# Kernel tuning notes

Measured on AMD Instinct MI355X. Metric: run time of the kernel, lower is better.

Reference implementation:

```python
import jax, jax.numpy as jnp
import numpy as np

R = 32          # voxel resolution (init kwarg)
EPS = 0.0       # init kwarg eps


def _norm_coords(coords):
    # coords: [B, 3, N]
    nc = coords - coords.mean(axis=2, keepdims=True)
    # L2 norm over xyz (dim=1), max over points (dim=2)
    denom = jnp.linalg.norm(nc, axis=1, keepdims=True).max(axis=2, keepdims=True) * 2.0 + EPS
    nc = nc / denom + 0.5
    return jnp.clip(nc * R, 0.0, R - 1)  # [B, 3, N] in [0, R-1]


def setup_inputs() -> dict:
    key = jax.random.key(0)
    k1, k2 = jax.random.split(key)
    features = jax.random.normal(k1, (8, 64, 65536), dtype=jnp.float32)
    coords = jax.random.normal(k2, (8, 3, 65536), dtype=jnp.float32)
    return {"features": features, "coords": coords}


def reference(features, coords):
    # features: [B, C, N], coords: [B, 3, N]
    nc = _norm_coords(coords)
    vox = jnp.round(nc).astype(jnp.int32)                      # [B, 3, N]
    flat = (vox[:, 0] * R + vox[:, 1]) * R + vox[:, 2]         # [B, N] flat voxel ids

    def per_batch(f, idx):
        # f: [C, N], idx: [N] -> scatter-mean into R^3 voxels
        sums = jax.ops.segment_sum(f.T, idx, num_segments=R ** 3)            # [R^3, C]
        cnt = jax.ops.segment_sum(jnp.ones(idx.shape, jnp.float32), idx,
                                  num_segments=R ** 3)                        # [R^3]
        return (sums / jnp.maximum(cnt, 1.0)[:, None]).T                      # [C, R^3]

    vox_feat = jax.vmap(per_batch)(features, flat)             # [B, C, R^3]
    B, C = features.shape[0], features.shape[1]
    return vox_feat.reshape(B, C, R, R, R), nc
```

## Files before the change

kernel.cpp:

```cpp
#include <hip/hip_runtime.h>

#define RR 32
#define R3 32768
#define NPTS 65536
#define NCH 64
#define NB 8


__global__ void mean_kernel(const float* __restrict__ coords, double* __restrict__ sums) {
    int b = blockIdx.y;
    int tid = blockIdx.x * blockDim.x + threadIdx.x;
    int stride = gridDim.x * blockDim.x;
    const float* cb = coords + (size_t)b * 3 * NPTS;
    double sx = 0.0, sy = 0.0, sz = 0.0;
    for (int n = tid; n < NPTS; n += stride) {
        sx += cb[n];
        sy += cb[NPTS + n];
        sz += cb[2 * NPTS + n];
    }
    for (int off = 32; off > 0; off >>= 1) {
        sx += __shfl_down(sx, off);
        sy += __shfl_down(sy, off);
        sz += __shfl_down(sz, off);
    }
    if ((threadIdx.x & 63) == 0) {
        atomicAdd(&sums[b * 3 + 0], sx);
        atomicAdd(&sums[b * 3 + 1], sy);
        atomicAdd(&sums[b * 3 + 2], sz);
    }
}

__global__ void maxnorm_kernel(const float* __restrict__ coords,
                               const double* __restrict__ sums,
                               unsigned* __restrict__ maxbits) {
    int b = blockIdx.y;
    float mx = (float)(sums[b * 3 + 0] * (1.0 / NPTS));
    float my = (float)(sums[b * 3 + 1] * (1.0 / NPTS));
    float mz = (float)(sums[b * 3 + 2] * (1.0 / NPTS));
    int tid = blockIdx.x * blockDim.x + threadIdx.x;
    int stride = gridDim.x * blockDim.x;
    const float* cb = coords + (size_t)b * 3 * NPTS;
    float m = 0.0f;
    for (int n = tid; n < NPTS; n += stride) {
        float dx = cb[n] - mx;
        float dy = cb[NPTS + n] - my;
        float dz = cb[2 * NPTS + n] - mz;
        m = fmaxf(m, dx * dx + dy * dy + dz * dz);
    }
    for (int off = 32; off > 0; off >>= 1) {
        m = fmaxf(m, __shfl_down(m, off));
    }
    if ((threadIdx.x & 63) == 0) {
        atomicMax(&maxbits[b], __float_as_uint(m));
    }
}


__global__ void scatter_vm_kernel(const float* __restrict__ feats,
                                  const float* __restrict__ coords,
                                  const double* __restrict__ sums,
                                  const unsigned* __restrict__ maxbits,
                                  float* __restrict__ ws_vox,
                                  float* __restrict__ ncout,
                                  float* __restrict__ cnt) {
    __shared__ float tile[64][65];
    __shared__ int   sflat[64];

    int b  = blockIdx.y;
    int n0 = blockIdx.x * 64;
    int t  = threadIdx.x;

    if (t < 64) {
        int n = n0 + t;
        float mx = (float)(sums[b * 3 + 0] * (1.0 / NPTS));
        float my = (float)(sums[b * 3 + 1] * (1.0 / NPTS));
        float mz = (float)(sums[b * 3 + 2] * (1.0 / NPTS));
        float denom = 2.0f * sqrtf(__uint_as_float(maxbits[b]));
        const float* cb = coords + (size_t)b * 3 * NPTS;
        float dx = cb[n] - mx;
        float dy = cb[NPTS + n] - my;
        float dz = cb[2 * NPTS + n] - mz;
        float qx = fminf(fmaxf((dx / denom + 0.5f) * 32.0f, 0.0f), 31.0f);
        float qy = fminf(fmaxf((dy / denom + 0.5f) * 32.0f, 0.0f), 31.0f);
        float qz = fminf(fmaxf((dz / denom + 0.5f) * 32.0f, 0.0f), 31.0f);
        float* nb_ = ncout + (size_t)b * 3 * NPTS;
        nb_[n] = qx;
        nb_[NPTS + n] = qy;
        nb_[2 * NPTS + n] = qz;
        int flat = ((int)rintf(qx) * RR + (int)rintf(qy)) * RR + (int)rintf(qz);
        sflat[t] = flat;
        atomicAdd(&cnt[b * R3 + flat], 1.0f);
    }

    const float* fb = feats + (size_t)b * NCH * NPTS + n0;
    int i = t & 63;
    int c0 = t >> 6;
#pragma unroll
    for (int iter = 0; iter < 16; iter++) {
        int c = iter * 4 + c0;
        tile[i][c] = fb[(size_t)c * NPTS + i];
    }
    __syncthreads();

    int wave = t >> 6;
    int lane = t & 63;
#pragma unroll
    for (int k = 0; k < 16; k++) {
        int p = wave * 16 + k;
        float v = tile[p][lane];
        size_t base = ((size_t)b * R3 + sflat[p]) * NCH;
        atomicAdd(&ws_vox[base + lane], v);
    }
}

__global__ void normalize_t_kernel(const float* __restrict__ ws_vox,
                                   const float* __restrict__ cnt,
                                   float* __restrict__ voxout) {
    __shared__ float tile[64][65];
    __shared__ float cinv[64];

    int b  = blockIdx.y;
    int v0 = blockIdx.x * 64;
    int t  = threadIdx.x;

    if (t < 64) {
        float c = cnt[b * R3 + v0 + t];
        cinv[t] = 1.0f / fmaxf(c, 1.0f);
    }

    const float* src = ws_vox + ((size_t)b * R3 + v0) * NCH;
    int c = t & 63;
    int vi0 = t >> 6;
#pragma unroll
    for (int iter = 0; iter < 16; iter++) {
        int vi = iter * 4 + vi0;
        tile[c][vi] = src[(size_t)vi * NCH + c];
    }
    __syncthreads();

    float* dst = voxout + (size_t)b * NCH * R3 + v0;
    int vi = t & 63;
    int cc0 = t >> 6;
#pragma unroll
    for (int iter = 0; iter < 16; iter++) {
        int cc = iter * 4 + cc0;
        dst[(size_t)cc * R3 + vi] = tile[cc][vi] * cinv[vi];
    }
}


__global__ void scatter_kernel(const float* __restrict__ feats,
                               const float* __restrict__ coords,
                               const double* __restrict__ sums,
                               const unsigned* __restrict__ maxbits,
                               float* __restrict__ voxsum,
                               float* __restrict__ ncout,
                               float* __restrict__ cnt) {
    int b = blockIdx.y;
    int n = blockIdx.x * blockDim.x + threadIdx.x;
    float mx = (float)(sums[b * 3 + 0] * (1.0 / NPTS));
    float my = (float)(sums[b * 3 + 1] * (1.0 / NPTS));
    float mz = (float)(sums[b * 3 + 2] * (1.0 / NPTS));
    float denom = 2.0f * sqrtf(__uint_as_float(maxbits[b]));
    const float* cb = coords + (size_t)b * 3 * NPTS;
    float dx = cb[n] - mx;
    float dy = cb[NPTS + n] - my;
    float dz = cb[2 * NPTS + n] - mz;
    float qx = fminf(fmaxf((dx / denom + 0.5f) * 32.0f, 0.0f), 31.0f);
    float qy = fminf(fmaxf((dy / denom + 0.5f) * 32.0f, 0.0f), 31.0f);
    float qz = fminf(fmaxf((dz / denom + 0.5f) * 32.0f, 0.0f), 31.0f);
    float* nb_ = ncout + (size_t)b * 3 * NPTS;
    nb_[n] = qx;
    nb_[NPTS + n] = qy;
    nb_[2 * NPTS + n] = qz;
    int flat = ((int)rintf(qx) * RR + (int)rintf(qy)) * RR + (int)rintf(qz);
    atomicAdd(&cnt[b * R3 + flat], 1.0f);
    const float* fb = feats + (size_t)b * NCH * NPTS + n;
    float* ob = voxsum + (size_t)b * NCH * R3 + flat;
#pragma unroll 8
    for (int c = 0; c < NCH; c++) {
        atomicAdd(ob + (size_t)c * R3, fb[(size_t)c * NPTS]);
    }
}

__global__ void normalize_kernel(float* __restrict__ voxsum, const float* __restrict__ cnt) {
    int i = blockIdx.x * blockDim.x + threadIdx.x;
    int b = i >> 15;
    int v = i & (R3 - 1);
    float inv = 1.0f / fmaxf(cnt[i], 1.0f);
    float* ob = voxsum + ((size_t)b * NCH) * R3 + v;
#pragma unroll 8
    for (int c2 = 0; c2 < NCH; c2++) {
        ob[(size_t)c2 * R3] *= inv;
    }
}

extern "C" void kernel_launch(void* const* d_in, const int* in_sizes, int n_in,
                              void* d_out, int out_size, void* d_ws, size_t ws_size,
                              hipStream_t stream) {
    const float* feats  = (const float*)d_in[0];
    const float* coords = (const float*)d_in[1];
    float* out = (float*)d_out;
    float* voxout = out;
    float* ncout  = out + (size_t)NB * NCH * R3;

    double*   sums    = (double*)d_ws;
    unsigned* maxbits = (unsigned*)((char*)d_ws + 192);
    const size_t off_cnt = 4096;
    const size_t cnt_bytes = (size_t)NB * R3 * sizeof(float);
    const size_t off_vox = off_cnt + cnt_bytes;
    const size_t vox_bytes = (size_t)NB * R3 * NCH * sizeof(float);
    float* cnt    = (float*)((char*)d_ws + off_cnt);
    float* ws_vox = (float*)((char*)d_ws + off_vox);

    mean_kernel   <<<dim3(32, NB), 256, 0, stream>>>(coords, sums);

    if (ws_size >= off_vox + vox_bytes) {
        hipMemsetAsync((char*)d_ws + 192, 0, 32, stream);
        hipMemsetAsync(d_ws, 0, 192, stream);
        hipMemsetAsync((char*)d_ws + off_cnt, 0, cnt_bytes, stream);
        hipMemsetAsync((char*)d_ws + off_vox, 0, vox_bytes, stream);
        mean_kernel   <<<dim3(32, NB), 256, 0, stream>>>(coords, sums);
        maxnorm_kernel<<<dim3(32, NB), 256, 0, stream>>>(coords, sums, maxbits);
        scatter_vm_kernel<<<dim3(NPTS / 64, NB), 256, 0, stream>>>(
            feats, coords, sums, maxbits, ws_vox, ncout, cnt);
        normalize_t_kernel<<<dim3(R3 / 64, NB), 256, 0, stream>>>(ws_vox, cnt, voxout);
    } else {
        hipMemsetAsync(d_ws, 0, off_cnt + cnt_bytes, stream);
        hipMemsetAsync(voxout, 0, (size_t)NB * NCH * R3 * sizeof(float), stream);
        mean_kernel   <<<dim3(32, NB), 256, 0, stream>>>(coords, sums);
        maxnorm_kernel<<<dim3(32, NB), 256, 0, stream>>>(coords, sums, maxbits);
        scatter_kernel<<<dim3(NPTS / 256, NB), 256, 0, stream>>>(feats, coords, sums, maxbits,
                                                                 voxout, ncout, cnt);
        normalize_kernel<<<(NB * R3) / 256, 256, 0, stream>>>(voxout, cnt);
    }
}
```

Baseline: 399.2 us.

## Replace float atomic scatter with counting-sort and atomic-free gather reduction

```diff
diff --git a/kernel.cpp b/kernel.cpp
--- a/kernel.cpp
+++ b/kernel.cpp
@@ -56,6 +56,147 @@
 }
 
 
+__global__ void nc_vid_kernel(const float* __restrict__ coords,
+                              const double* __restrict__ sums,
+                              const unsigned* __restrict__ maxbits,
+                              float* __restrict__ ncout,
+                              int* __restrict__ vid,
+                              unsigned* __restrict__ cnt) {
+    int b = blockIdx.y;
+    int n = blockIdx.x * blockDim.x + threadIdx.x;
+    float mx = (float)(sums[b * 3 + 0] * (1.0 / NPTS));
+    float my = (float)(sums[b * 3 + 1] * (1.0 / NPTS));
+    float mz = (float)(sums[b * 3 + 2] * (1.0 / NPTS));
+    float denom = 2.0f * sqrtf(__uint_as_float(maxbits[b]));
+    const float* cb = coords + (size_t)b * 3 * NPTS;
+    float dx = cb[n] - mx;
+    float dy = cb[NPTS + n] - my;
+    float dz = cb[2 * NPTS + n] - mz;
+    float qx = fminf(fmaxf((dx / denom + 0.5f) * 32.0f, 0.0f), 31.0f);
+    float qy = fminf(fmaxf((dy / denom + 0.5f) * 32.0f, 0.0f), 31.0f);
+    float qz = fminf(fmaxf((dz / denom + 0.5f) * 32.0f, 0.0f), 31.0f);
+    float* nb_ = ncout + (size_t)b * 3 * NPTS;
+    nb_[n] = qx;
+    nb_[NPTS + n] = qy;
+    nb_[2 * NPTS + n] = qz;
+    int flat = ((int)rintf(qx) * RR + (int)rintf(qy)) * RR + (int)rintf(qz);
+    vid[b * NPTS + n] = flat;
+    atomicAdd(&cnt[b * R3 + flat], 1u);
+}
+
+__global__ void scan_kernel(const unsigned* __restrict__ cnt,
+                            unsigned* __restrict__ off,
+                            unsigned* __restrict__ cursor) {
+    __shared__ unsigned ls[1024];
+    int b = blockIdx.x;
+    int t = threadIdx.x;
+    const unsigned* c = cnt + b * R3;
+    int base = t * 32;
+    unsigned v[32];
+    unsigned s = 0;
+#pragma unroll
+    for (int k = 0; k < 32; k++) {
+        unsigned x = c[base + k];
+        v[k] = s;
+        s += x;
+    }
+    ls[t] = s;
+    __syncthreads();
+    for (int d = 1; d < 1024; d <<= 1) {
+        unsigned x = (t >= d) ? ls[t - d] : 0u;
+        __syncthreads();
+        ls[t] += x;
+        __syncthreads();
+    }
+    unsigned chunk_excl = (t == 0) ? 0u : ls[t - 1];
+#pragma unroll
+    for (int k = 0; k < 32; k++) {
+        unsigned o = chunk_excl + v[k];
+        off[b * R3 + base + k] = o;
+        cursor[b * R3 + base + k] = o;
+    }
+}
+
+__global__ void scatter_idx_kernel(const int* __restrict__ vid,
+                                   unsigned* __restrict__ cursor,
+                                   int* __restrict__ order) {
+    int b = blockIdx.y;
+    int n = blockIdx.x * blockDim.x + threadIdx.x;
+    int flat = vid[b * NPTS + n];
+    unsigned pos = atomicAdd(&cursor[b * R3 + flat], 1u);
+    order[b * NPTS + pos] = n;
+}
+
+__global__ void transpose_feat_kernel(const float* __restrict__ feats,
+                                      float* __restrict__ ft) {
+    __shared__ float tile[64][65];
+    int b  = blockIdx.y;
+    int n0 = blockIdx.x * 64;
+    int t  = threadIdx.x;
+    const float* fb = feats + (size_t)b * NCH * NPTS + n0;
+    int i  = t & 63;
+    int c0 = t >> 6;
+#pragma unroll
+    for (int iter = 0; iter < 16; iter++) {
+        int c = iter * 4 + c0;
+        tile[i][c] = fb[(size_t)c * NPTS + i];
+    }
+    __syncthreads();
+    float* dst = ft + ((size_t)b * NPTS + n0) * NCH;
+    int c  = t & 63;
+    int p0 = t >> 6;
+#pragma unroll
+    for (int iter = 0; iter < 16; iter++) {
+        int p = iter * 4 + p0;
+        dst[(size_t)p * NCH + c] = tile[p][c];
+    }
+}
+
+__global__ void gather_kernel(const float* __restrict__ ft,
+                              const int* __restrict__ order,
+                              const unsigned* __restrict__ off,
+                              const unsigned* __restrict__ cnt,
+                              float* __restrict__ voxout) {
+    __shared__ float tile[64][65];
+    int b    = blockIdx.y;
+    int v0   = blockIdx.x * 64;
+    int t    = threadIdx.x;
+    int wave = t >> 6;
+    int lane = t & 63;
+
+    const float* fb = ft + ((size_t)b * NPTS) * NCH + lane;
+    const int* ordb = order + b * NPTS;
+
+#pragma unroll
+    for (int k = 0; k < 16; k++) {
+        int vloc = wave * 16 + k;
+        int v = v0 + vloc;
+        unsigned start = off[b * R3 + v];
+        unsigned m = cnt[b * R3 + v];
+        float s0 = 0.0f, s1 = 0.0f;
+        unsigned j = 0;
+        for (; j + 2 <= m; j += 2) {
+            int i0 = ordb[start + j];
+            int i1 = ordb[start + j + 1];
+            s0 += fb[(size_t)i0 * NCH];
+            s1 += fb[(size_t)i1 * NCH];
+        }
+        if (j < m) s0 += fb[(size_t)ordb[start + j] * NCH];
+        tile[vloc][lane] = (s0 + s1) / fmaxf((float)m, 1.0f);
+    }
+    __syncthreads();
+
+    float* dst = voxout + (size_t)b * NCH * R3 + v0;
+    int vi = t & 63;
+    int c0 = t >> 6;
+#pragma unroll
+    for (int iter = 0; iter < 16; iter++) {
+        int c = iter * 4 + c0;
+        dst[(size_t)c * R3 + vi] = tile[vi][c];
+    }
+}
+
+
 __global__ void scatter_vm_kernel(const float* __restrict__ feats,
                                   const float* __restrict__ coords,
                                   const double* __restrict__ sums,
@@ -65,11 +206,9 @@
                                   float* __restrict__ cnt) {
     __shared__ float tile[64][65];
     __shared__ int   sflat[64];
-
     int b  = blockIdx.y;
     int n0 = blockIdx.x * 64;
     int t  = threadIdx.x;
-
     if (t < 64) {
         int n = n0 + t;
         float mx = (float)(sums[b * 3 + 0] * (1.0 / NPTS));
@@ -91,7 +230,6 @@
         sflat[t] = flat;
         atomicAdd(&cnt[b * R3 + flat], 1.0f);
     }
-
     const float* fb = feats + (size_t)b * NCH * NPTS + n0;
     int i = t & 63;
     int c0 = t >> 6;
@@ -101,7 +239,6 @@
         tile[i][c] = fb[(size_t)c * NPTS + i];
     }
     __syncthreads();
-
     int wave = t >> 6;
     int lane = t & 63;
 #pragma unroll
@@ -118,18 +255,12 @@
                                    float* __restrict__ voxout) {
     __shared__ float tile[64][65];
     __shared__ float cinv[64];
-
     int b  = blockIdx.y;
     int v0 = blockIdx.x * 64;
     int t  = threadIdx.x;
-
-    if (t < 64) {
-        float c = cnt[b * R3 + v0 + t];
-        cinv[t] = 1.0f / fmaxf(c, 1.0f);
-    }
-
+    if (t < 64) cinv[t] = 1.0f / fmaxf(cnt[b * R3 + v0 + t], 1.0f);
     const float* src = ws_vox + ((size_t)b * R3 + v0) * NCH;
-    int c = t & 63;
+    int c   = t & 63;
     int vi0 = t >> 6;
 #pragma unroll
     for (int iter = 0; iter < 16; iter++) {
@@ -137,61 +268,13 @@
         tile[c][vi] = src[(size_t)vi * NCH + c];
     }
     __syncthreads();
-
     float* dst = voxout + (size_t)b * NCH * R3 + v0;
-    int vi = t & 63;
+    int vi  = t & 63;
     int cc0 = t >> 6;
 #pragma unroll
     for (int iter = 0; iter < 16; iter++) {
         int cc = iter * 4 + cc0;
         dst[(size_t)cc * R3 + vi] = tile[cc][vi] * cinv[vi];
-    }
-}
-
-
-__global__ void scatter_kernel(const float* __restrict__ feats,
-                               const float* __restrict__ coords,
-                               const double* __restrict__ sums,
-                               const unsigned* __restrict__ maxbits,
-                               float* __restrict__ voxsum,
-                               float* __restrict__ ncout,
-                               float* __restrict__ cnt) {
-    int b = blockIdx.y;
-    int n = blockIdx.x * blockDim.x + threadIdx.x;
-    float mx = (float)(sums[b * 3 + 0] * (1.0 / NPTS));
-    float my = (float)(sums[b * 3 + 1] * (1.0 / NPTS));
-    float mz = (float)(sums[b * 3 + 2] * (1.0 / NPTS));
-    float denom = 2.0f * sqrtf(__uint_as_float(maxbits[b]));
-    const float* cb = coords + (size_t)b * 3 * NPTS;
-    float dx = cb[n] - mx;
-    float dy = cb[NPTS + n] - my;
-    float dz = cb[2 * NPTS + n] - mz;
-    float qx = fminf(fmaxf((dx / denom + 0.5f) * 32.0f, 0.0f), 31.0f);
-    float qy = fminf(fmaxf((dy / denom + 0.5f) * 32.0f, 0.0f), 31.0f);
-    float qz = fminf(fmaxf((dz / denom + 0.5f) * 32.0f, 0.0f), 31.0f);
-    float* nb_ = ncout + (size_t)b * 3 * NPTS;
-    nb_[n] = qx;
-    nb_[NPTS + n] = qy;
-    nb_[2 * NPTS + n] = qz;
-    int flat = ((int)rintf(qx) * RR + (int)rintf(qy)) * RR + (int)rintf(qz);
-    atomicAdd(&cnt[b * R3 + flat], 1.0f);
-    const float* fb = feats + (size_t)b * NCH * NPTS + n;
-    float* ob = voxsum + (size_t)b * NCH * R3 + flat;
-#pragma unroll 8
-    for (int c = 0; c < NCH; c++) {
-        atomicAdd(ob + (size_t)c * R3, fb[(size_t)c * NPTS]);
-    }
-}
-
-__global__ void normalize_kernel(float* __restrict__ voxsum, const float* __restrict__ cnt) {
-    int i = blockIdx.x * blockDim.x + threadIdx.x;
-    int b = i >> 15;
-    int v = i & (R3 - 1);
-    float inv = 1.0f / fmaxf(cnt[i], 1.0f);
-    float* ob = voxsum + ((size_t)b * NCH) * R3 + v;
-#pragma unroll 8
-    for (int c2 = 0; c2 < NCH; c2++) {
-        ob[(size_t)c2 * R3] *= inv;
     }
 }
 
@@ -206,32 +289,49 @@
 
     double*   sums    = (double*)d_ws;
     unsigned* maxbits = (unsigned*)((char*)d_ws + 192);
+
     const size_t off_cnt = 4096;
-    const size_t cnt_bytes = (size_t)NB * R3 * sizeof(float);
+    const size_t cnt_bytes = (size_t)NB * R3 * 4;
+    const size_t off_off = off_cnt + cnt_bytes;
+    const size_t off_cur = off_off + cnt_bytes;
+    const size_t off_vid = off_cur + cnt_bytes;
+    const size_t vid_bytes = (size_t)NB * NPTS * 4;
+    const size_t off_ord = off_vid + vid_bytes;
+    const size_t off_ft  = off_ord + vid_bytes;
+    const size_t ft_bytes = (size_t)NB * NPTS * NCH * 4;
+    const size_t need_sort = off_ft + ft_bytes;
+
     const size_t off_vox = off_cnt + cnt_bytes;
-    const size_t vox_bytes = (size_t)NB * R3 * NCH * sizeof(float);
-    float* cnt    = (float*)((char*)d_ws + off_cnt);
-    float* ws_vox = (float*)((char*)d_ws + off_vox);
-
-    mean_kernel   <<<dim3(32, NB), 256, 0, stream>>>(coords, sums);
-
-    if (ws_size >= off_vox + vox_bytes) {
-        hipMemsetAsync((char*)d_ws + 192, 0, 32, stream);
-        hipMemsetAsync(d_ws, 0, 192, stream);
-        hipMemsetAsync((char*)d_ws + off_cnt, 0, cnt_bytes, stream);
+    const size_t vox_bytes = (size_t)NB * R3 * NCH * 4;
+    const size_t need_vm = off_vox + vox_bytes;
+
+    if (ws_size >= need_sort) {
+        unsigned* cnt    = (unsigned*)((char*)d_ws + off_cnt);
+        unsigned* off    = (unsigned*)((char*)d_ws + off_off);
+        unsigned* cursor = (unsigned*)((char*)d_ws + off_cur);
+        int*      vid    = (int*)((char*)d_ws + off_vid);
+        int*      order  = (int*)((char*)d_ws + off_ord);
+        float*    ft     = (float*)((char*)d_ws + off_ft);
+
+        hipMemsetAsync(d_ws, 0, off_cnt + cnt_bytes, stream);
+
+        mean_kernel   <<<dim3(64, NB), 256, 0, stream>>>(coords, sums);
+        maxnorm_kernel<<<dim3(64, NB), 256, 0, stream>>>(coords, sums, maxbits);
+        nc_vid_kernel <<<dim3(NPTS / 256, NB), 256, 0, stream>>>(coords, sums, maxbits,
+                                                                 ncout, vid, cnt);
+        scan_kernel   <<<NB, 1024, 0, stream>>>(cnt, off, cursor);
+        scatter_idx_kernel<<<dim3(NPTS / 256, NB), 256, 0, stream>>>(vid, cursor, order);
+        transpose_feat_kernel<<<dim3(NPTS / 64, NB), 256, 0, stream>>>(feats, ft);
+        gather_kernel <<<dim3(R3 / 64, NB), 256, 0, stream>>>(ft, order, off, cnt, voxout);
+    } else if (ws_size >= need_vm) {
+        float* cntf   = (float*)((char*)d_ws + off_cnt);
+        float* ws_vox = (float*)((char*)d_ws + off_vox);
+        hipMemsetAsync(d_ws, 0, off_cnt + cnt_bytes, stream);
         hipMemsetAsync((char*)d_ws + off_vox, 0, vox_bytes, stream);
-        mean_kernel   <<<dim3(32, NB), 256, 0, stream>>>(coords, sums);
-        maxnorm_kernel<<<dim3(32, NB), 256, 0, stream>>>(coords, sums, maxbits);
+        mean_kernel   <<<dim3(64, NB), 256, 0, stream>>>(coords, sums);
+        maxnorm_kernel<<<dim3(64, NB), 256, 0, stream>>>(coords, sums, maxbits);
         scatter_vm_kernel<<<dim3(NPTS / 64, NB), 256, 0, stream>>>(
-            feats, coords, sums, maxbits, ws_vox, ncout, cnt);
-        normalize_t_kernel<<<dim3(R3 / 64, NB), 256, 0, stream>>>(ws_vox, cnt, voxout);
-    } else {
-        hipMemsetAsync(d_ws, 0, off_cnt + cnt_bytes, stream);
-        hipMemsetAsync(voxout, 0, (size_t)NB * NCH * R3 * sizeof(float), stream);
-        mean_kernel   <<<dim3(32, NB), 256, 0, stream>>>(coords, sums);
-        maxnorm_kernel<<<dim3(32, NB), 256, 0, stream>>>(coords, sums, maxbits);
-        scatter_kernel<<<dim3(NPTS / 256, NB), 256, 0, stream>>>(feats, coords, sums, maxbits,
-                                                                 voxout, ncout, cnt);
-        normalize_kernel<<<(NB * R3) / 256, 256, 0, stream>>>(voxout, cnt);
-    }
-}
+            feats, coords, sums, maxbits, ws_vox, ncout, cntf);
+        normalize_t_kernel<<<dim3(R3 / 64, NB), 256, 0, stream>>>(ws_vox, cntf, voxout);
+    }
+}
```

New measurement: 761.9 us. 1.91x slower.
